# Performance work log

Hardware: AMD Instinct MI355X
Metric: run time of the kernel (lower is better)

Reference implementation:

```python
import jax, jax.numpy as jnp
import numpy as np

T = 800_000      # total words across all sentences
S = 2048         # total sentences
B = 32           # number of sequences (documents)
M = 64           # max sentences per sequence (here exactly 64 each)
D_IN = 256
D_OUT = 128


def setup_inputs() -> dict:
    key = jax.random.key(0)
    k_tok, k_w, k_b = jax.random.split(key, 3)
    rng = np.random.default_rng(0)

    # ragged word counts per sentence, each >= 1, summing to T
    lengths = rng.multinomial(T - S, np.full(S, 1.0 / S)) + 1
    seg_ids = jnp.asarray(np.repeat(np.arange(S, dtype=np.int32), lengths))

    # sentence -> (document, position-in-document)
    sent_batch = jnp.asarray(np.repeat(np.arange(B, dtype=np.int32), M))
    sent_pos = jnp.asarray(np.tile(np.arange(M, dtype=np.int32), B))

    tokens = jax.random.normal(k_tok, (T, D_IN), dtype=jnp.float32)
    # nn.Linear default init scale ~ 1/sqrt(in_features)
    bound = 1.0 / np.sqrt(D_IN)
    weight = jax.random.uniform(k_w, (D_OUT, D_IN), jnp.float32, -bound, bound)
    bias = jax.random.uniform(k_b, (D_OUT,), jnp.float32, -bound, bound)
    return {"tokens": tokens, "weight": weight, "bias": bias,
            "seg_ids": seg_ids, "sent_batch": sent_batch, "sent_pos": sent_pos}


def reference(tokens, weight, bias, seg_ids, sent_batch, sent_pos):
    # per-word linear: [T, D_OUT]
    h = tokens @ weight.T + bias
    # max-pool words within each sentence: [S, D_OUT]
    sent = jax.ops.segment_max(h, seg_ids, num_segments=S)
    # pad_sequence(batch_first=True) -> zero-padded [B, M, D_OUT]
    out = jnp.zeros((B, M, D_OUT), dtype=h.dtype).at[sent_batch, sent_pos].set(sent)
    return out
```

## Files before the change

### kernel.cpp

```cpp
#include <hip/hip_runtime.h>
#include <hip/hip_bf16.h>

#define T_WORDS 800000
#define S_SENT 2048
#define DIN 256
#define DOUT 128
#define CHUNK 32

typedef short bf16x8 __attribute__((ext_vector_type(8)));
typedef float f32x4 __attribute__((ext_vector_type(4)));

__device__ __forceinline__ unsigned short f2bf(float f) {
  unsigned int u = __builtin_bit_cast(unsigned int, f);
  u += 0x7fffu + ((u >> 16) & 1u);
  return (unsigned short)(u >> 16);
}

__global__ void prep_kernel(const float* __restrict__ weight,
                            const int* __restrict__ seg,
                            unsigned short* __restrict__ wsB,
                            int* __restrict__ starts) {
  int tid = blockIdx.x * blockDim.x + threadIdx.x;
  int stride = gridDim.x * blockDim.x;
  for (int j = tid; j < DOUT * DIN; j += stride)
    wsB[j] = f2bf(weight[j]);
  for (int j = tid; j < T_WORDS; j += stride) {
    if (j == 0) {
      starts[seg[0]] = 0;
    } else {
      int s1 = seg[j], s0 = seg[j - 1];
      if (s1 != s0) starts[s1] = j;
    }
  }
}

__global__ __launch_bounds__(256) void pool_kernel(
    const float* __restrict__ tokens,
    const float* __restrict__ bias,
    const unsigned short* __restrict__ wsB,
    const int* __restrict__ starts,
    const int* __restrict__ sent_batch,
    const int* __restrict__ sent_pos,
    float* __restrict__ out) {
  __shared__ alignas(16) unsigned short Alds[2][CHUNK * DIN];

  const int s = blockIdx.x;
  const int start = starts[s];
  const int end = (s == S_SENT - 1) ? T_WORDS : starts[s + 1];
  const int lane = (int)(threadIdx.x & 63);
  const int wv = (int)(threadIdx.x >> 6);

  bf16x8 bfrag[2][8];
#pragma unroll
  for (int n = 0; n < 2; ++n) {
    const int col = 32 * wv + 16 * n + (lane & 15);
    const unsigned short* wrow = wsB + col * DIN + 8 * (lane >> 4);
#pragma unroll
    for (int kk = 0; kk < 8; ++kk)
      bfrag[n][kk] = *(const bf16x8*)(wrow + 32 * kk);
  }

  const int srow0 = (int)(threadIdx.x >> 5);
  const int sk8 = (int)(threadIdx.x & 31);

  float runmax0 = -INFINITY, runmax1 = -INFINITY;
  float4 pf[4][2];

#define ISSUE_LOADS(WBASE)                                                    \
  {                                                                           \
    _Pragma("unroll") for (int it = 0; it < 4; ++it) {                        \
      int word = (WBASE) + srow0 + 8 * it;                                    \
      if (word < end) {                                                       \
        const float4* src =                                                   \
            (const float4*)(tokens + (size_t)word * DIN + sk8 * 8);           \
        pf[it][0] = src[0];                                                   \
        pf[it][1] = src[1];                                                   \
      }                                                                       \
    }                                                                         \
  }

#define WRITE_STAGE(BUF)                                                      \
  {                                                                           \
    _Pragma("unroll") for (int it = 0; it < 4; ++it) {                        \
      int row = srow0 + 8 * it;                                               \
      float4 f0 = pf[it][0], f1 = pf[it][1];                                  \
      bf16x8 v;                                                               \
      v[0] = (short)f2bf(f0.x); v[1] = (short)f2bf(f0.y);                     \
      v[2] = (short)f2bf(f0.z); v[3] = (short)f2bf(f0.w);                     \
      v[4] = (short)f2bf(f1.x); v[5] = (short)f2bf(f1.y);                     \
      v[6] = (short)f2bf(f1.z); v[7] = (short)f2bf(f1.w);                     \
      int idx = (row * DIN + sk8 * 8) ^ ((row & 7) << 3);                     \
      *(bf16x8*)&Alds[BUF][idx] = v;                                          \
    }                                                                         \
  }

#define COMPUTE(BUF, WBASE)                                                   \
  {                                                                           \
    _Pragma("unroll") for (int m = 0; m < 2; ++m) {                           \
      f32x4 acc0 = (f32x4){0.f, 0.f, 0.f, 0.f};                               \
      f32x4 acc1 = (f32x4){0.f, 0.f, 0.f, 0.f};                               \
      const int arow = 16 * m + (lane & 15);                                  \
      const int abase = arow * DIN + 8 * (lane >> 4);                         \
      const int axor = (lane & 7) << 3;                                       \
      _Pragma("unroll") for (int kk = 0; kk < 8; ++kk) {                      \
        bf16x8 a = *(const bf16x8*)&Alds[BUF][(abase + 32 * kk) ^ axor];      \
        acc0 = __builtin_amdgcn_mfma_f32_16x16x32_bf16(a, bfrag[0][kk], acc0, \
                                                       0, 0, 0);              \
        acc1 = __builtin_amdgcn_mfma_f32_16x16x32_bf16(a, bfrag[1][kk], acc1, \
                                                       0, 0, 0);              \
      }                                                                       \
      const int w0 = (WBASE) + 16 * m + 4 * (lane >> 4);                      \
      _Pragma("unroll") for (int r = 0; r < 4; ++r) {                         \
        if (w0 + r < end) {                                                   \
          runmax0 = fmaxf(runmax0, acc0[r]);                                  \
          runmax1 = fmaxf(runmax1, acc1[r]);                                  \
        }                                                                     \
      }                                                                       \
    }                                                                         \
  }

  const int nch = (end - start + CHUNK - 1) / CHUNK;

  ISSUE_LOADS(start)
  WRITE_STAGE(0)
  __syncthreads();

  for (int c = 0; c < nch; ++c) {
    const int cur = c & 1;
    const int wbase = start + c * CHUNK;
    if (c + 1 < nch) ISSUE_LOADS(wbase + CHUNK)
    COMPUTE(cur, wbase)
    if (c + 1 < nch) WRITE_STAGE(cur ^ 1)
    __syncthreads();
  }

  runmax0 = fmaxf(runmax0, __shfl_xor(runmax0, 16, 64));
  runmax0 = fmaxf(runmax0, __shfl_xor(runmax0, 32, 64));
  runmax1 = fmaxf(runmax1, __shfl_xor(runmax1, 16, 64));
  runmax1 = fmaxf(runmax1, __shfl_xor(runmax1, 32, 64));

  if (lane < 16) {
    const int sb = sent_batch[s], sp = sent_pos[s];
    float* o = out + ((size_t)sb * 64 + sp) * DOUT;
    const int c0 = 32 * wv + lane;
    o[c0] = runmax0 + bias[c0];
    o[c0 + 16] = runmax1 + bias[c0 + 16];
  }
}

extern "C" void kernel_launch(void* const* d_in, const int* in_sizes, int n_in,
                              void* d_out, int out_size, void* d_ws, size_t ws_size,
                              hipStream_t stream) {
  const float* tokens = (const float*)d_in[0];
  const float* weight = (const float*)d_in[1];
  const float* bias   = (const float*)d_in[2];
  const int* seg      = (const int*)d_in[3];
  const int* sbatch   = (const int*)d_in[4];
  const int* spos     = (const int*)d_in[5];
  float* out = (float*)d_out;

  unsigned short* wsB = (unsigned short*)d_ws;
  int* starts = (int*)((char*)d_ws + DOUT * DIN * sizeof(unsigned short));

  prep_kernel<<<512, 256, 0, stream>>>(weight, seg, wsB, starts);
  pool_kernel<<<S_SENT, 256, 0, stream>>>(tokens, bias, wsB, starts, sbatch, spos, out);
}
```

Baseline: 153.5 us.

## Use 512-thread blocks with two-deep register prefetch and lighter barriers

Blocks grow from 256 to 512 threads, so each wave now owns 16 output columns instead of 32. Each thread stages one token row segment of 16 floats per chunk. Two register buffers prefetch chunks c+1 and c+2 while chunk c is computed from LDS, which keeps more global loads in flight per block. __syncthreads is replaced by an explicit lgkmcnt wait plus s_barrier. The risks are higher register pressure under the new launch bounds and the cost of syncing 8 waves per barrier.

After: 162.9 us. 1.06x slower.

```diff
diff --git a/kernel.cpp b/kernel.cpp
--- a/kernel.cpp
+++ b/kernel.cpp
@@ -6,6 +6,7 @@
 #define DIN 256
 #define DOUT 128
 #define CHUNK 32
+#define BLK 512
 
 typedef short bf16x8 __attribute__((ext_vector_type(8)));
 typedef float f32x4 __attribute__((ext_vector_type(4)));
@@ -34,7 +35,7 @@
   }
 }
 
-__global__ __launch_bounds__(256) void pool_kernel(
+__global__ __launch_bounds__(BLK, 4) void pool_kernel(
     const float* __restrict__ tokens,
     const float* __restrict__ bias,
     const unsigned short* __restrict__ wsB,
@@ -50,101 +51,103 @@
   const int lane = (int)(threadIdx.x & 63);
   const int wv = (int)(threadIdx.x >> 6);
 
-  bf16x8 bfrag[2][8];
-#pragma unroll
-  for (int n = 0; n < 2; ++n) {
-    const int col = 32 * wv + 16 * n + (lane & 15);
+  bf16x8 bfrag[8];
+  {
+    const int col = 16 * wv + (lane & 15);
     const unsigned short* wrow = wsB + col * DIN + 8 * (lane >> 4);
 #pragma unroll
     for (int kk = 0; kk < 8; ++kk)
-      bfrag[n][kk] = *(const bf16x8*)(wrow + 32 * kk);
+      bfrag[kk] = *(const bf16x8*)(wrow + 32 * kk);
   }
 
-  const int srow0 = (int)(threadIdx.x >> 5);
-  const int sk8 = (int)(threadIdx.x & 31);
+  const int srow = (int)(threadIdx.x >> 4);
+  const int skseg = (int)(threadIdx.x & 15);
+  const int sw = (srow & 7) << 3;
+  const int sidx0 = srow * DIN + skseg * 16;
 
-  float runmax0 = -INFINITY, runmax1 = -INFINITY;
-  float4 pf[4][2];
+  float runmax = -INFINITY;
+  float4 pA0, pA1, pA2, pA3, pB0, pB1, pB2, pB3;
 
-#define ISSUE_LOADS(WBASE)                                                    \
+#define ISSUE(P0, P1, P2, P3, WBASE)                                          \
   {                                                                           \
-    _Pragma("unroll") for (int it = 0; it < 4; ++it) {                        \
-      int word = (WBASE) + srow0 + 8 * it;                                    \
-      if (word < end) {                                                       \
-        const float4* src =                                                   \
-            (const float4*)(tokens + (size_t)word * DIN + sk8 * 8);           \
-        pf[it][0] = src[0];                                                   \
-        pf[it][1] = src[1];                                                   \
-      }                                                                       \
+    int word = (WBASE) + srow;                                                \
+    if (word < end) {                                                         \
+      const float4* src =                                                     \
+          (const float4*)(tokens + (size_t)word * DIN + skseg * 16);          \
+      P0 = src[0]; P1 = src[1]; P2 = src[2]; P3 = src[3];                     \
     }                                                                         \
   }
 
-#define WRITE_STAGE(BUF)                                                      \
+#define WRITE(P0, P1, P2, P3, BUF)                                            \
   {                                                                           \
-    _Pragma("unroll") for (int it = 0; it < 4; ++it) {                        \
-      int row = srow0 + 8 * it;                                               \
-      float4 f0 = pf[it][0], f1 = pf[it][1];                                  \
-      bf16x8 v;                                                               \
-      v[0] = (short)f2bf(f0.x); v[1] = (short)f2bf(f0.y);                     \
-      v[2] = (short)f2bf(f0.z); v[3] = (short)f2bf(f0.w);                     \
-      v[4] = (short)f2bf(f1.x); v[5] = (short)f2bf(f1.y);                     \
-      v[6] = (short)f2bf(f1.z); v[7] = (short)f2bf(f1.w);                     \
-      int idx = (row * DIN + sk8 * 8) ^ ((row & 7) << 3);                     \
-      *(bf16x8*)&Alds[BUF][idx] = v;                                          \
-    }                                                                         \
+    bf16x8 v0, v1;                                                            \
+    v0[0] = (short)f2bf(P0.x); v0[1] = (short)f2bf(P0.y);                     \
+    v0[2] = (short)f2bf(P0.z); v0[3] = (short)f2bf(P0.w);                     \
+    v0[4] = (short)f2bf(P1.x); v0[5] = (short)f2bf(P1.y);                     \
+    v0[6] = (short)f2bf(P1.z); v0[7] = (short)f2bf(P1.w);                     \
+    v1[0] = (short)f2bf(P2.x); v1[1] = (short)f2bf(P2.y);                     \
+    v1[2] = (short)f2bf(P2.z); v1[3] = (short)f2bf(P2.w);                     \
+    v1[4] = (short)f2bf(P3.x); v1[5] = (short)f2bf(P3.y);                     \
+    v1[6] = (short)f2bf(P3.z); v1[7] = (short)f2bf(P3.w);                     \
+    *(bf16x8*)&Alds[BUF][sidx0 ^ sw] = v0;                                    \
+    *(bf16x8*)&Alds[BUF][(sidx0 + 8) ^ sw] = v1;                              \
   }
 
 #define COMPUTE(BUF, WBASE)                                                   \
   {                                                                           \
     _Pragma("unroll") for (int m = 0; m < 2; ++m) {                           \
-      f32x4 acc0 = (f32x4){0.f, 0.f, 0.f, 0.f};                               \
-      f32x4 acc1 = (f32x4){0.f, 0.f, 0.f, 0.f};                               \
+      f32x4 acc = (f32x4){0.f, 0.f, 0.f, 0.f};                                \
       const int arow = 16 * m + (lane & 15);                                  \
       const int abase = arow * DIN + 8 * (lane >> 4);                         \
       const int axor = (lane & 7) << 3;                                       \
       _Pragma("unroll") for (int kk = 0; kk < 8; ++kk) {                      \
         bf16x8 a = *(const bf16x8*)&Alds[BUF][(abase + 32 * kk) ^ axor];      \
-        acc0 = __builtin_amdgcn_mfma_f32_16x16x32_bf16(a, bfrag[0][kk], acc0, \
-                                                       0, 0, 0);              \
-        acc1 = __builtin_amdgcn_mfma_f32_16x16x32_bf16(a, bfrag[1][kk], acc1, \
-                                                       0, 0, 0);              \
+        acc = __builtin_amdgcn_mfma_f32_16x16x32_bf16(a, bfrag[kk], acc,      \
+                                                      0, 0, 0);               \
       }                                                                       \
       const int w0 = (WBASE) + 16 * m + 4 * (lane >> 4);                      \
       _Pragma("unroll") for (int r = 0; r < 4; ++r) {                         \
-        if (w0 + r < end) {                                                   \
-          runmax0 = fmaxf(runmax0, acc0[r]);                                  \
-          runmax1 = fmaxf(runmax1, acc1[r]);                                  \
-        }                                                                     \
+        if (w0 + r < end) runmax = fmaxf(runmax, acc[r]);                     \
       }                                                                       \
     }                                                                         \
   }
 
+#define BAR()                                                                 \
+  {                                                                           \
+    asm volatile("s_waitcnt lgkmcnt(0)" ::: "memory");                        \
+    __builtin_amdgcn_s_barrier();                                             \
+  }
+
   const int nch = (end - start + CHUNK - 1) / CHUNK;
 
-  ISSUE_LOADS(start)
-  WRITE_STAGE(0)
-  __syncthreads();
+  ISSUE(pA0, pA1, pA2, pA3, start)
+  if (nch > 1) ISSUE(pB0, pB1, pB2, pB3, start + CHUNK)
+  WRITE(pA0, pA1, pA2, pA3, 0)
+  BAR()
 
-  for (int c = 0; c < nch; ++c) {
-    const int cur = c & 1;
-    const int wbase = start + c * CHUNK;
-    if (c + 1 < nch) ISSUE_LOADS(wbase + CHUNK)
-    COMPUTE(cur, wbase)
-    if (c + 1 < nch) WRITE_STAGE(cur ^ 1)
-    __syncthreads();
+  int c = 0;
+  while (true) {
+    COMPUTE(0, start + c * CHUNK)
+    if (c + 2 < nch) ISSUE(pA0, pA1, pA2, pA3, start + (c + 2) * CHUNK)
+    if (c + 1 < nch) WRITE(pB0, pB1, pB2, pB3, 1)
+    BAR()
+    if (++c >= nch) break;
+
+    COMPUTE(1, start + c * CHUNK)
+    if (c + 2 < nch) ISSUE(pB0, pB1, pB2, pB3, start + (c + 2) * CHUNK)
+    if (c + 1 < nch) WRITE(pA0, pA1, pA2, pA3, 0)
+    BAR()
+    if (++c >= nch) break;
   }
 
-  runmax0 = fmaxf(runmax0, __shfl_xor(runmax0, 16, 64));
-  runmax0 = fmaxf(runmax0, __shfl_xor(runmax0, 32, 64));
-  runmax1 = fmaxf(runmax1, __shfl_xor(runmax1, 16, 64));
-  runmax1 = fmaxf(runmax1, __shfl_xor(runmax1, 32, 64));
+  runmax = fmaxf(runmax, __shfl_xor(runmax, 16, 64));
+  runmax = fmaxf(runmax, __shfl_xor(runmax, 32, 64));
 
   if (lane < 16) {
     const int sb = sent_batch[s], sp = sent_pos[s];
     float* o = out + ((size_t)sb * 64 + sp) * DOUT;
-    const int c0 = 32 * wv + lane;
-    o[c0] = runmax0 + bias[c0];
-    o[c0 + 16] = runmax1 + bias[c0 + 16];
+    const int c0 = 16 * wv + lane;
+    o[c0] = runmax + bias[c0];
   }
 }
 
@@ -163,5 +166,5 @@
   int* starts = (int*)((char*)d_ws + DOUT * DIN * sizeof(unsigned short));
 
   prep_kernel<<<512, 256, 0, stream>>>(weight, seg, wsB, starts);
-  pool_kernel<<<S_SENT, 256, 0, stream>>>(tokens, bias, wsB, starts, sbatch, spos, out);
+  pool_kernel<<<S_SENT, BLK, 0, stream>>>(tokens, bias, wsB, starts, sbatch, spos, out);
 }
```

## Deepen token prefetch pipeline and pad tail rows with -inf to drop masking

Applied to the files above, without the earlier changes.

Restructures the per-sentence loop so global loads for chunk c+2 are issued while chunk c is computed and chunk c+1 is staged into LDS. The two LDS buffers are unrolled explicitly, and the full __syncthreads is replaced by an lgkmcnt wait plus s_barrier. Out-of-range rows are filled with bf16 -inf, so the per-row bounds check in the max reduction goes away. This relies on the resulting NaN/-inf MFMA outputs being ignored by fmaxf. The change also uses packed bf16x2 conversion and sets a launch-bounds occupancy hint of 3 blocks per CU.

Result: slower. 160.8 us (+4.8%).

```diff
diff --git a/kernel.cpp b/kernel.cpp
--- a/kernel.cpp
+++ b/kernel.cpp
@@ -9,6 +9,15 @@
 
 typedef short bf16x8 __attribute__((ext_vector_type(8)));
 typedef float f32x4 __attribute__((ext_vector_type(4)));
+
+union V16 { bf16x8 v; unsigned int u[4]; };
+
+__device__ __forceinline__ unsigned int pk2(float lo, float hi) {
+  __hip_bfloat162 h = __float22bfloat162_rn(float2{lo, hi});
+  unsigned int u;
+  __builtin_memcpy(&u, &h, sizeof(u));
+  return u;
+}
 
 __device__ __forceinline__ unsigned short f2bf(float f) {
   unsigned int u = __builtin_bit_cast(unsigned int, f);
@@ -34,7 +43,7 @@
   }
 }
 
-__global__ __launch_bounds__(256) void pool_kernel(
+__global__ __launch_bounds__(256, 3) void pool_kernel(
     const float* __restrict__ tokens,
     const float* __restrict__ bias,
     const unsigned short* __restrict__ wsB,
@@ -66,7 +75,7 @@
   float runmax0 = -INFINITY, runmax1 = -INFINITY;
   float4 pf[4][2];
 
-#define ISSUE_LOADS(WBASE)                                                    \
+#define ISSUE(WBASE)                                                          \
   {                                                                           \
     _Pragma("unroll") for (int it = 0; it < 4; ++it) {                        \
       int word = (WBASE) + srow0 + 8 * it;                                    \
@@ -79,22 +88,22 @@
     }                                                                         \
   }
 
-#define WRITE_STAGE(BUF)                                                      \
+#define WRITE(WBASE, BUF)                                                     \
   {                                                                           \
     _Pragma("unroll") for (int it = 0; it < 4; ++it) {                        \
       int row = srow0 + 8 * it;                                               \
-      float4 f0 = pf[it][0], f1 = pf[it][1];                                  \
-      bf16x8 v;                                                               \
-      v[0] = (short)f2bf(f0.x); v[1] = (short)f2bf(f0.y);                     \
-      v[2] = (short)f2bf(f0.z); v[3] = (short)f2bf(f0.w);                     \
-      v[4] = (short)f2bf(f1.x); v[5] = (short)f2bf(f1.y);                     \
-      v[6] = (short)f2bf(f1.z); v[7] = (short)f2bf(f1.w);                     \
+      bool valid = (WBASE) + row < end;                                       \
+      V16 w;                                                                  \
+      w.u[0] = valid ? pk2(pf[it][0].x, pf[it][0].y) : 0xFF80FF80u;           \
+      w.u[1] = valid ? pk2(pf[it][0].z, pf[it][0].w) : 0xFF80FF80u;           \
+      w.u[2] = valid ? pk2(pf[it][1].x, pf[it][1].y) : 0xFF80FF80u;           \
+      w.u[3] = valid ? pk2(pf[it][1].z, pf[it][1].w) : 0xFF80FF80u;           \
       int idx = (row * DIN + sk8 * 8) ^ ((row & 7) << 3);                     \
-      *(bf16x8*)&Alds[BUF][idx] = v;                                          \
+      *(bf16x8*)&Alds[BUF][idx] = w.v;                                        \
     }                                                                         \
   }
 
-#define COMPUTE(BUF, WBASE)                                                   \
+#define COMPUTE(BUF)                                                          \
   {                                                                           \
     _Pragma("unroll") for (int m = 0; m < 2; ++m) {                           \
       f32x4 acc0 = (f32x4){0.f, 0.f, 0.f, 0.f};                               \
@@ -109,29 +118,41 @@
         acc1 = __builtin_amdgcn_mfma_f32_16x16x32_bf16(a, bfrag[1][kk], acc1, \
                                                        0, 0, 0);              \
       }                                                                       \
-      const int w0 = (WBASE) + 16 * m + 4 * (lane >> 4);                      \
-      _Pragma("unroll") for (int r = 0; r < 4; ++r) {                         \
-        if (w0 + r < end) {                                                   \
-          runmax0 = fmaxf(runmax0, acc0[r]);                                  \
-          runmax1 = fmaxf(runmax1, acc1[r]);                                  \
-        }                                                                     \
-      }                                                                       \
+      runmax0 = fmaxf(runmax0, fmaxf(fmaxf(acc0[0], acc0[1]),                 \
+                                     fmaxf(acc0[2], acc0[3])));               \
+      runmax1 = fmaxf(runmax1, fmaxf(fmaxf(acc1[0], acc1[1]),                 \
+                                     fmaxf(acc1[2], acc1[3])));               \
     }                                                                         \
+  }
+
+#define BAR()                                                                 \
+  {                                                                           \
+    asm volatile("s_waitcnt lgkmcnt(0)" ::: "memory");                        \
+    __builtin_amdgcn_s_barrier();                                             \
   }
 
   const int nch = (end - start + CHUNK - 1) / CHUNK;
 
-  ISSUE_LOADS(start)
-  WRITE_STAGE(0)
-  __syncthreads();
+  ISSUE(start)
+  WRITE(start, 0)
+  if (nch > 1) ISSUE(start + CHUNK)
+  BAR()
 
-  for (int c = 0; c < nch; ++c) {
-    const int cur = c & 1;
-    const int wbase = start + c * CHUNK;
-    if (c + 1 < nch) ISSUE_LOADS(wbase + CHUNK)
-    COMPUTE(cur, wbase)
-    if (c + 1 < nch) WRITE_STAGE(cur ^ 1)
-    __syncthreads();
+  int c = 0;
+  while (true) {
+    int wb = start + c * CHUNK;
+    if (c + 1 < nch) WRITE(wb + CHUNK, 1)
+    if (c + 2 < nch) ISSUE(wb + 2 * CHUNK)
+    COMPUTE(0)
+    BAR()
+    if (++c >= nch) break;
+
+    wb = start + c * CHUNK;
+    if (c + 1 < nch) WRITE(wb + CHUNK, 0)
+    if (c + 2 < nch) ISSUE(wb + 2 * CHUNK)
+    COMPUTE(1)
+    BAR()
+    if (++c >= nch) break;
   }
 
   runmax0 = fmaxf(runmax0, __shfl_xor(runmax0, 16, 64));
```
